# Kernel tuning notes

Hardware: AMD Instinct MI355X
Metric: run time of the kernel (lower is better)

The kernel has to match this reference:

```python
import jax, jax.numpy as jnp
import numpy as np

GRID_NUM = 3  # pykan 'grid' (number of intervals)
K = 3         # spline order

def bspline_basis(x, grid, k):
    # Cox-de Boor recursion, matching pykan B_batch with a shared extended grid.
    # x: (N, Din); grid: (G,) extended grid with G = GRID_NUM + 2*k + 1
    x = x[..., None]  # (N, Din, 1)
    B = ((x >= grid[:-1]) & (x < grid[1:])).astype(x.dtype)  # (N, Din, G-1)
    for p in range(1, k + 1):
        left = (x - grid[:-(p + 1)]) / (grid[p:-1] - grid[:-(p + 1)])
        right = (grid[p + 1:] - x) / (grid[p + 1:] - grid[1:-p])
        B = left * B[..., :-1] + right * B[..., 1:]
    return B  # (N, Din, GRID_NUM + k)

def setup_inputs() -> dict:
    key = jax.random.key(0)
    k1, k2, k3 = jax.random.split(key, 3)
    Bsz, S, Din, Dout = 4, 2048, 768, 768
    x = jax.random.normal(k1, (Bsz, S, Din), dtype=jnp.float32)
    # noise-scale-like init for spline coefficients (noise_scale=0.1)
    coef = (0.1 / GRID_NUM) * jax.random.normal(k2, (Dout, Din, GRID_NUM + K), dtype=jnp.float32)
    inv_sqrt_in = np.float32(1.0 / np.sqrt(Din))
    scale_base = inv_sqrt_in + 0.1 * inv_sqrt_in * jax.random.normal(k3, (Dout, Din), dtype=jnp.float32)
    scale_sp = jnp.ones((Dout, Din), dtype=jnp.float32)
    bias = jnp.zeros((Dout,), dtype=jnp.float32)
    return {"x": x, "coef": coef, "scale_base": scale_base, "scale_sp": scale_sp, "bias": bias}

def reference(x, coef, scale_base, scale_sp, bias):
    # x: (B, S, Din) -> flatten tokens as the original module does
    Bsz, S, Din = x.shape
    xf = x.reshape(-1, Din)  # (N, Din)
    # extended grid: linspace(-1,1,GRID_NUM+1) extended by K points each side (h = 2/GRID_NUM)
    h = 2.0 / GRID_NUM
    grid = jnp.arange(-K, GRID_NUM + K + 1, dtype=x.dtype) * h - 1.0  # (GRID_NUM + 2K + 1,)
    basis = bspline_basis(xf, grid, K)  # (N, Din, GRID_NUM+K)
    # per-edge activation: scale_base*silu(x) + scale_sp*spline(x); mask==1; symbolic branch==0
    base = jax.nn.silu(xf) @ scale_base.T  # (N, Dout)
    spline = jnp.einsum('nim,oim->no', basis, scale_sp[:, :, None] * coef)  # (N, Dout)
    out = base + spline + bias  # bias from pykan biases[l].weight
    return out.reshape(Bsz, S, -1)
```

## Files before the change

### kernel.cpp

```cpp
#include <hip/hip_runtime.h>


typedef _Float16 f16;
typedef __attribute__((ext_vector_type(4))) _Float16 f16x4;
typedef __attribute__((ext_vector_type(8))) _Float16 f16x8;
typedef __attribute__((ext_vector_type(4))) float f32x4;

#define NTOK 8192
#define DIN 768
#define DOUT 768
#define KAUG 5376
#define BM 128
#define BN 128
#define BK 32
#define KT (KAUG / BK)

typedef __attribute__((address_space(1))) void gvoid;
typedef __attribute__((address_space(3))) void lvoid;

__device__ __forceinline__ void spline6(float xv, float* __restrict__ B, float& s) {
  s = xv / (1.0f + __expf(-xv));
  const float h = 2.0f / 3.0f;
  float Bb[9];
#pragma unroll
  for (int g = 0; g < 9; ++g) {
    float t0 = (float)(g - 3) * h - 1.0f;
    float t1 = (float)(g - 2) * h - 1.0f;
    Bb[g] = (xv >= t0 && xv < t1) ? 1.0f : 0.0f;
  }
#pragma unroll
  for (int p = 1; p <= 3; ++p) {
    float inv = 1.0f / ((float)p * h);
#pragma unroll
    for (int j = 0; j < 8; ++j) {
      if (j < 9 - p) {
        float tj = (float)(j - 3) * h - 1.0f;
        float tjp1 = (float)(j + p + 1 - 3) * h - 1.0f;
        Bb[j] = (xv - tj) * inv * Bb[j] + (tjp1 - xv) * inv * Bb[j + 1];
      }
    }
  }
#pragma unroll
  for (int m = 0; m < 6; ++m) B[m] = Bb[m];
}

__global__ __launch_bounds__(256) void build_A(const float* __restrict__ x,
                                               f16* __restrict__ Aa) {
  int idx = (blockIdx.x * 256 + threadIdx.x) * 4;
  float4 xv = *(const float4*)(x + idx);
  int n = idx / DIN;
  int i = idx - n * DIN;

  float B0[6], B1[6], B2[6], B3[6];
  float s0, s1, s2, s3;
  spline6(xv.x, B0, s0);
  spline6(xv.y, B1, s1);
  spline6(xv.z, B2, s2);
  spline6(xv.w, B3, s3);

  size_t base = (size_t)n * KAUG + i;
  f16x4 sv = {(f16)s0, (f16)s1, (f16)s2, (f16)s3};
  *(f16x4*)(Aa + base) = sv;
#pragma unroll
  for (int m = 0; m < 6; ++m) {
    f16x4 bv = {(f16)B0[m], (f16)B1[m], (f16)B2[m], (f16)B3[m]};
    *(f16x4*)(Aa + base + (size_t)(m + 1) * DIN) = bv;
  }
}

__global__ __launch_bounds__(256) void build_W(const float* __restrict__ sb,
                                               const float* __restrict__ ssp,
                                               const float* __restrict__ coef,
                                               f16* __restrict__ Wa) {
  int idx = blockIdx.x * 256 + threadIdx.x;
  float b = sb[idx];
  float sp = ssp[idx];
  int o = idx / DIN;
  int i = idx - o * DIN;
  size_t base = (size_t)o * KAUG + i;
  Wa[base] = (f16)b;
#pragma unroll
  for (int m = 0; m < 6; ++m)
    Wa[base + (size_t)(m + 1) * DIN] = (f16)(sp * coef[(size_t)idx * 6 + m]);
}

__global__ __launch_bounds__(256) void kan_gemm(const f16* __restrict__ A,
                                                const f16* __restrict__ W,
                                                const float* __restrict__ bias,
                                                float* __restrict__ out) {
  __shared__ alignas(16) f16 As0[BM * BK];
  __shared__ alignas(16) f16 As1[BM * BK];
  __shared__ alignas(16) f16 Bs0[BN * BK];
  __shared__ alignas(16) f16 Bs1[BN * BK];

  const int tid = threadIdx.x;
  const int wave = tid >> 6;
  const int lane = tid & 63;
  const int m0 = blockIdx.y * BM;
  const int n0 = blockIdx.x * BN;
  const int wm = (wave >> 1) * 64;
  const int wn = (wave & 1) * 64;
  const int r = lane & 15;
  const int q = lane >> 4;

  f32x4 acc[4][4] = {};

  const int c0 = wave * 64 + lane;
  const int rowA0 = c0 >> 2, kb0 = c0 & 3;
  const int c1 = c0 + 256;
  const int rowA1 = c1 >> 2, kb1 = c1 & 3;

  const f16* gA0 = A + (size_t)(m0 + rowA0) * KAUG + kb0 * 8;
  const f16* gA1 = A + (size_t)(m0 + rowA1) * KAUG + kb1 * 8;
  const f16* gB0 = W + (size_t)(n0 + rowA0) * KAUG + kb0 * 8;
  const f16* gB1 = W + (size_t)(n0 + rowA1) * KAUG + kb1 * 8;

  const int wo = wave * 512;

#define STAGE(AS, BS, ktile)                                                             \
  do {                                                                                   \
    const int koff = (ktile)*BK;                                                         \
    __builtin_amdgcn_global_load_lds((gvoid*)(gA0 + koff), (lvoid*)(AS + wo), 16, 0, 0); \
    __builtin_amdgcn_global_load_lds((gvoid*)(gA1 + koff), (lvoid*)(AS + wo + 2048), 16, \
                                     0, 0);                                              \
    __builtin_amdgcn_global_load_lds((gvoid*)(gB0 + koff), (lvoid*)(BS + wo), 16, 0, 0); \
    __builtin_amdgcn_global_load_lds((gvoid*)(gB1 + koff), (lvoid*)(BS + wo + 2048), 16, \
                                     0, 0);                                              \
  } while (0)

#define COMPUTE(AS, BS)                                                                  \
  do {                                                                                   \
    f16x8 af[4], bf[4];                                                                  \
    _Pragma("unroll") for (int mi = 0; mi < 4; ++mi) af[mi] =                            \
        *(const f16x8*)&AS[(wm + mi * 16 + r) * BK + q * 8];                             \
    _Pragma("unroll") for (int ni = 0; ni < 4; ++ni) bf[ni] =                            \
        *(const f16x8*)&BS[(wn + ni * 16 + r) * BK + q * 8];                             \
    _Pragma("unroll") for (int mi = 0; mi < 4; ++mi) _Pragma("unroll") for (int ni = 0;  \
                                                                            ni < 4;     \
                                                                            ++ni)       \
        acc[mi][ni] =                                                                    \
        __builtin_amdgcn_mfma_f32_16x16x32_f16(af[mi], bf[ni], acc[mi][ni], 0, 0, 0);    \
  } while (0)

  STAGE(As0, Bs0, 0);
  __syncthreads();

  for (int kt = 0; kt < KT; kt += 2) {
    STAGE(As1, Bs1, kt + 1);
    COMPUTE(As0, Bs0);
    __syncthreads();
    if (kt + 2 < KT) STAGE(As0, Bs0, kt + 2);
    COMPUTE(As1, Bs1);
    __syncthreads();
  }

#undef STAGE
#undef COMPUTE

#pragma unroll
  for (int mi = 0; mi < 4; ++mi) {
#pragma unroll
    for (int ni = 0; ni < 4; ++ni) {
      const int gcol = n0 + wn + ni * 16 + r;
      const float bv = bias[gcol];
#pragma unroll
      for (int rg = 0; rg < 4; ++rg) {
        const int grow = m0 + wm + mi * 16 + q * 4 + rg;
        out[(size_t)grow * DOUT + gcol] = acc[mi][ni][rg] + bv;
      }
    }
  }
}

extern "C" void kernel_launch(void* const* d_in, const int* in_sizes, int n_in,
                              void* d_out, int out_size, void* d_ws, size_t ws_size,
                              hipStream_t stream) {
  const float* x = (const float*)d_in[0];
  const float* coef = (const float*)d_in[1];
  const float* scale_base = (const float*)d_in[2];
  const float* scale_sp = (const float*)d_in[3];
  const float* bias = (const float*)d_in[4];
  float* out = (float*)d_out;

  f16* Aa = (f16*)d_ws;
  f16* Wa = (f16*)((char*)d_ws + (size_t)NTOK * KAUG * 2);

  build_A<<<(NTOK * DIN) / (256 * 4), 256, 0, stream>>>(x, Aa);
  build_W<<<(DOUT * DIN) / 256, 256, 0, stream>>>(scale_base, scale_sp, coef, Wa);
  kan_gemm<<<dim3(DOUT / BN, NTOK / BM), 256, 0, stream>>>(Aa, Wa, bias, out);
}
```

Before: 221.9 us.

## Split-K GEMM in halves with atomic accumulation, XCD-aware tile mapping, LDS swizzle

The K dimension is split in two so the GEMM launches 768 blocks instead of 384, giving better occupancy across CUs. A separate kernel initializes the output with bias, and partial sums are combined with unsafe atomic float adds. Block IDs are remapped so that each half of K maps to a group of XCDs, which is meant to improve L2 locality. An XOR swizzle on the LDS k-chunk is added to reduce bank conflicts. In exchange the kernel pays for atomic read-modify-write traffic on the output and one extra launch.

Measured after the change: 222.6 us. Within noise of the previous version (+0.3%).

```diff
diff --git a/kernel.cpp b/kernel.cpp
--- a/kernel.cpp
+++ b/kernel.cpp
@@ -13,7 +13,8 @@
 #define BM 128
 #define BN 128
 #define BK 32
-#define KT (KAUG / BK)
+#define KHALF (KAUG / 2)
+#define KHSTEPS (KHALF / BK)
 
 typedef __attribute__((address_space(1))) void gvoid;
 typedef __attribute__((address_space(3))) void lvoid;
@@ -84,9 +85,14 @@
     Wa[base + (size_t)(m + 1) * DIN] = (f16)(sp * coef[(size_t)idx * 6 + m]);
 }
 
+__global__ __launch_bounds__(256) void out_init(const float* __restrict__ bias,
+                                                float* __restrict__ out) {
+  int idx = blockIdx.x * 256 + threadIdx.x;
+  ((float4*)out)[idx] = ((const float4*)bias)[idx % (DOUT / 4)];
+}
+
 __global__ __launch_bounds__(256) void kan_gemm(const f16* __restrict__ A,
                                                 const f16* __restrict__ W,
-                                                const float* __restrict__ bias,
                                                 float* __restrict__ out) {
   __shared__ alignas(16) f16 As0[BM * BK];
   __shared__ alignas(16) f16 As1[BM * BK];
@@ -96,8 +102,16 @@
   const int tid = threadIdx.x;
   const int wave = tid >> 6;
   const int lane = tid & 63;
-  const int m0 = blockIdx.y * BM;
-  const int n0 = blockIdx.x * BN;
+
+  const int bid = blockIdx.x;
+  const int xcd = bid & 7;
+  const int j = bid >> 3;
+  const int half = xcd >> 2;
+  const int t = (xcd & 3) * 96 + j;
+  const int m0 = (t / 6) * BM;
+  const int n0 = (t % 6) * BN;
+  const size_t k0 = (size_t)half * KHALF;
+
   const int wm = (wave >> 1) * 64;
   const int wn = (wave & 1) * 64;
   const int r = lane & 15;
@@ -106,50 +120,52 @@
   f32x4 acc[4][4] = {};
 
   const int c0 = wave * 64 + lane;
-  const int rowA0 = c0 >> 2, kb0 = c0 & 3;
   const int c1 = c0 + 256;
-  const int rowA1 = c1 >> 2, kb1 = c1 & 3;
-
-  const f16* gA0 = A + (size_t)(m0 + rowA0) * KAUG + kb0 * 8;
-  const f16* gA1 = A + (size_t)(m0 + rowA1) * KAUG + kb1 * 8;
-  const f16* gB0 = W + (size_t)(n0 + rowA0) * KAUG + kb0 * 8;
-  const f16* gB1 = W + (size_t)(n0 + rowA1) * KAUG + kb1 * 8;
+  const int row0 = c0 >> 2, kb0 = (c0 & 3) ^ ((c0 >> 3) & 3);
+  const int row1 = c1 >> 2, kb1 = (c1 & 3) ^ ((c1 >> 3) & 3);
+
+  const f16* gA0 = A + (size_t)(m0 + row0) * KAUG + k0 + kb0 * 8;
+  const f16* gA1 = A + (size_t)(m0 + row1) * KAUG + k0 + kb1 * 8;
+  const f16* gB0 = W + (size_t)(n0 + row0) * KAUG + k0 + kb0 * 8;
+  const f16* gB1 = W + (size_t)(n0 + row1) * KAUG + k0 + kb1 * 8;
 
   const int wo = wave * 512;
 
-#define STAGE(AS, BS, ktile)                                                             \
-  do {                                                                                   \
-    const int koff = (ktile)*BK;                                                         \
-    __builtin_amdgcn_global_load_lds((gvoid*)(gA0 + koff), (lvoid*)(AS + wo), 16, 0, 0); \
-    __builtin_amdgcn_global_load_lds((gvoid*)(gA1 + koff), (lvoid*)(AS + wo + 2048), 16, \
-                                     0, 0);                                              \
-    __builtin_amdgcn_global_load_lds((gvoid*)(gB0 + koff), (lvoid*)(BS + wo), 16, 0, 0); \
-    __builtin_amdgcn_global_load_lds((gvoid*)(gB1 + koff), (lvoid*)(BS + wo + 2048), 16, \
-                                     0, 0);                                              \
+#define STAGE(AS, BS, ktile)                                                              \
+  do {                                                                                    \
+    const int koff = (ktile)*BK;                                                          \
+    __builtin_amdgcn_global_load_lds((gvoid*)(gA0 + koff), (lvoid*)(AS + wo), 16, 0, 0);  \
+    __builtin_amdgcn_global_load_lds((gvoid*)(gA1 + koff), (lvoid*)(AS + wo + 2048), 16,  \
+                                     0, 0);                                               \
+    __builtin_amdgcn_global_load_lds((gvoid*)(gB0 + koff), (lvoid*)(BS + wo), 16, 0, 0);  \
+    __builtin_amdgcn_global_load_lds((gvoid*)(gB1 + koff), (lvoid*)(BS + wo + 2048), 16,  \
+                                     0, 0);                                               \
   } while (0)
 
-#define COMPUTE(AS, BS)                                                                  \
-  do {                                                                                   \
-    f16x8 af[4], bf[4];                                                                  \
-    _Pragma("unroll") for (int mi = 0; mi < 4; ++mi) af[mi] =                            \
-        *(const f16x8*)&AS[(wm + mi * 16 + r) * BK + q * 8];                             \
-    _Pragma("unroll") for (int ni = 0; ni < 4; ++ni) bf[ni] =                            \
-        *(const f16x8*)&BS[(wn + ni * 16 + r) * BK + q * 8];                             \
-    _Pragma("unroll") for (int mi = 0; mi < 4; ++mi) _Pragma("unroll") for (int ni = 0;  \
-                                                                            ni < 4;     \
-                                                                            ++ni)       \
-        acc[mi][ni] =                                                                    \
-        __builtin_amdgcn_mfma_f32_16x16x32_f16(af[mi], bf[ni], acc[mi][ni], 0, 0, 0);    \
+  const int sA = (q ^ ((r >> 1) & 3)) * 8;
+
+#define COMPUTE(AS, BS)                                                                   \
+  do {                                                                                    \
+    f16x8 af[4], bf[4];                                                                   \
+    _Pragma("unroll") for (int mi = 0; mi < 4; ++mi) af[mi] =                             \
+        *(const f16x8*)&AS[(wm + mi * 16 + r) * BK + sA];                                 \
+    _Pragma("unroll") for (int ni = 0; ni < 4; ++ni) bf[ni] =                             \
+        *(const f16x8*)&BS[(wn + ni * 16 + r) * BK + sA];                                 \
+    _Pragma("unroll") for (int mi = 0; mi < 4; ++mi) _Pragma("unroll") for (int ni = 0;   \
+                                                                            ni < 4;      \
+                                                                            ++ni)        \
+        acc[mi][ni] =                                                                     \
+        __builtin_amdgcn_mfma_f32_16x16x32_f16(af[mi], bf[ni], acc[mi][ni], 0, 0, 0);     \
   } while (0)
 
   STAGE(As0, Bs0, 0);
   __syncthreads();
 
-  for (int kt = 0; kt < KT; kt += 2) {
+  for (int kt = 0; kt < KHSTEPS; kt += 2) {
     STAGE(As1, Bs1, kt + 1);
     COMPUTE(As0, Bs0);
     __syncthreads();
-    if (kt + 2 < KT) STAGE(As0, Bs0, kt + 2);
+    if (kt + 2 < KHSTEPS) STAGE(As0, Bs0, kt + 2);
     COMPUTE(As1, Bs1);
     __syncthreads();
   }
@@ -162,11 +178,10 @@
 #pragma unroll
     for (int ni = 0; ni < 4; ++ni) {
       const int gcol = n0 + wn + ni * 16 + r;
-      const float bv = bias[gcol];
 #pragma unroll
       for (int rg = 0; rg < 4; ++rg) {
         const int grow = m0 + wm + mi * 16 + q * 4 + rg;
-        out[(size_t)grow * DOUT + gcol] = acc[mi][ni][rg] + bv;
+        unsafeAtomicAdd(&out[(size_t)grow * DOUT + gcol], acc[mi][ni][rg]);
       }
     }
   }
@@ -187,5 +202,6 @@
 
   build_A<<<(NTOK * DIN) / (256 * 4), 256, 0, stream>>>(x, Aa);
   build_W<<<(DOUT * DIN) / 256, 256, 0, stream>>>(scale_base, scale_sp, coef, Wa);
-  kan_gemm<<<dim3(DOUT / BN, NTOK / BM), 256, 0, stream>>>(Aa, Wa, bias, out);
-}
+  out_init<<<(NTOK * DOUT / 4) / 256, 256, 0, stream>>>(bias, out);
+  kan_gemm<<<768, 256, 0, stream>>>(Aa, Wa, out);
+}
```
